# Performance work log

Measured on AMD Instinct MI355X. Metric: run time of the kernel, lower is better.

Reference implementation:

```python
import jax, jax.numpy as jnp
import numpy as np

B, T, H, N_IN, N_OUT = 256, 1024, 512, 64, 64


def setup_inputs() -> dict:
    key = jax.random.key(0)
    k_x, k_w, k_win, k_wout = jax.random.split(key, 4)
    # nn.Linear(in, out, bias=False) weight has shape [out, in]
    X = jax.random.normal(k_x, (B, T, N_IN), dtype=jnp.float32)
    h0 = jnp.zeros((B, H), dtype=jnp.float32)
    W = jax.random.normal(k_w, (H, H), dtype=jnp.float32) / np.sqrt(H)
    W_in = jax.random.normal(k_win, (H, N_IN), dtype=jnp.float32) / np.sqrt(N_IN)
    W_out = jax.random.normal(k_wout, (N_OUT, H), dtype=jnp.float32) / np.sqrt(H)
    return {"X": X, "h0": h0, "W": W, "W_in": W_in, "W_out": W_out}


def reference(X, h0, W, W_in, W_out):
    # Precompute input projections for all timesteps in one big GEMM:
    # inp[b, t, h] = X[b, t, :] @ W_in.T  (same math as per-step W_in(x_t))
    inp = jnp.einsum("bti,hi->tbh", X, W_in)  # [T, B, H]

    def step(h, inp_t):
        h_next = jnp.tanh(h) @ W.T + inp_t  # [B, H]
        return h_next, h_next

    _, hidden = jax.lax.scan(step, h0, inp)  # hidden: [T, B, H]
    hidden = jnp.transpose(hidden, (1, 0, 2))  # [B, T, H]
    out = jnp.einsum("bth,oh->bto", hidden, W_out)  # [B, T, n_out]
    return out, hidden
```

## Files before the change

kernel.cpp:

```cpp
#include <hip/hip_runtime.h>
#include <stdint.h>

#define B_    256
#define T_    1024
#define H_    512
#define NIN_  64
#define NOUT_ 64

#define SC_NW   8
#define BBLK    4
#define HROW    528
#define KB_REG  10
#define KB_STR  6
#define SW_CHUNKS (SC_NW * KB_STR * 4 * 64)

typedef __attribute__((ext_vector_type(8))) short bf16x8;
typedef __attribute__((ext_vector_type(4))) float f32x4;

__device__ __forceinline__ short f2bf(float f) {
  uint32_t u = __float_as_uint(f);
  uint32_t r = (u + 0x7FFFu + ((u >> 16) & 1u)) >> 16;
  return (short)(r & 0xFFFFu);
}

__device__ __forceinline__ bf16x8 pack8(float4 lo, float4 hi) {
  bf16x8 s;
  s[0] = f2bf(lo.x); s[1] = f2bf(lo.y); s[2] = f2bf(lo.z); s[3] = f2bf(lo.w);
  s[4] = f2bf(hi.x); s[5] = f2bf(hi.y); s[6] = f2bf(hi.z); s[7] = f2bf(hi.w);
  return s;
}

__device__ __forceinline__ float fast_tanh(float x) {
  float e = __expf(2.0f * x);
  return 1.0f - __fdividef(2.0f, e + 1.0f);
}

__global__ __launch_bounds__(512) void wprep(
    const float* __restrict__ W, short* __restrict__ sw)
{
  const int c = blockIdx.x * 512 + threadIdx.x;
  if (c >= SW_CHUNKS) return;
  const int lane = c & 63;
  const int u    = c >> 6;
  const int jt   = u & 3;
  const int gw   = u >> 2;
  const int G    = gw % KB_STR;
  const int w    = gw / KB_STR;
  const int col  = 64 * w + 16 * jt + (lane & 15);
  const int k0   = 32 * (KB_REG + G) + (lane >> 4) * 8;
  const float4* p = reinterpret_cast<const float4*>(W + (size_t)col * H_ + k0);
  *reinterpret_cast<bf16x8*>(sw + (size_t)c * 8) = pack8(p[0], p[1]);
}

#define XP_BLOCKS 512
__global__ __launch_bounds__(512, 2) void xproj(
    const float* __restrict__ X, const float* __restrict__ Win,
    float* __restrict__ inp)
{
  const int tid  = threadIdx.x;
  const int lane = tid & 63;
  const int w    = tid >> 6;
  const int g    = lane >> 4;
  const int m    = lane & 15;

  bf16x8 Bf[2][4];
#pragma unroll
  for (int kb = 0; kb < 2; ++kb)
#pragma unroll
    for (int jt = 0; jt < 4; ++jt) {
      const int j = 64 * w + 16 * jt + m;
      const float4* p = reinterpret_cast<const float4*>(Win + (size_t)j * NIN_ + 32 * kb + 8 * g);
      Bf[kb][jt] = pack8(p[0], p[1]);
    }

  const int NTILES = (B_ * T_) / 16;
  const f32x4 zero = {0.f, 0.f, 0.f, 0.f};

  for (int tile = blockIdx.x; tile < NTILES; tile += XP_BLOCKS) {
    const size_t row0 = (size_t)tile * 16;
    f32x4 acc[4];
    {
      const float4* p = reinterpret_cast<const float4*>(X + (row0 + m) * NIN_ + 8 * g);
      const bf16x8 a = pack8(p[0], p[1]);
#pragma unroll
      for (int jt = 0; jt < 4; ++jt)
        acc[jt] = __builtin_amdgcn_mfma_f32_16x16x32_bf16(a, Bf[0][jt], zero, 0, 0, 0);
    }
    {
      const float4* p = reinterpret_cast<const float4*>(X + (row0 + m) * NIN_ + 32 + 8 * g);
      const bf16x8 a = pack8(p[0], p[1]);
#pragma unroll
      for (int jt = 0; jt < 4; ++jt)
        acc[jt] = __builtin_amdgcn_mfma_f32_16x16x32_bf16(a, Bf[1][jt], acc[jt], 0, 0, 0);
    }
#pragma unroll
    for (int jt = 0; jt < 4; ++jt)
#pragma unroll
      for (int r = 0; r < 4; ++r)
        inp[(row0 + 4 * g + r) * H_ + 64 * w + 16 * jt + m] = acc[jt][r];
  }
}

__global__
__attribute__((amdgpu_flat_work_group_size(512, 512), amdgpu_waves_per_eu(2, 2)))
void rnn_scan(
    const float* __restrict__ h0, const float* __restrict__ W,
    float* __restrict__ hid, const short* __restrict__ swbuf)
{
  __shared__ __align__(16) short hbuf[2][BBLK][HROW];

  const int tid  = threadIdx.x;
  const int lane = tid & 63;
  const int w    = tid >> 6;
  const int g    = lane >> 4;
  const int m    = lane & 15;
  const int b0   = blockIdx.x * BBLK;

  bf16x8 Wf[KB_REG][4];
#pragma unroll
  for (int kb = 0; kb < KB_REG; ++kb)
#pragma unroll
    for (int jt = 0; jt < 4; ++jt) {
      const int col = 64 * w + 16 * jt + m;
      const float4* p = reinterpret_cast<const float4*>(W + (size_t)col * H_ + 32 * kb + 8 * g);
      Wf[kb][jt] = pack8(p[0], p[1]);
    }

  for (int e = tid; e < BBLK * H_; e += SC_NW * 64) {
    const int r = e >> 9, k = e & (H_ - 1);
    hbuf[0][r][k] = f2bf(fast_tanh(h0[(size_t)(b0 + r) * H_ + k]));
  }

  const int mycol = 64 * w + 16 * g + m;
  float inp_cur[4];
#pragma unroll
  for (int r = 0; r < 4; ++r)
    inp_cur[r] = hid[((size_t)(b0 + r) * T_ + 0) * H_ + mycol];

  const int sbase = (w * KB_STR * 4) * 64 + lane;
  const bf16x8* SW = reinterpret_cast<const bf16x8*>(swbuf);
  bf16x8 s0[4], s1[4];
#pragma unroll
  for (int jt = 0; jt < 4; ++jt) s0[jt] = SW[sbase + (0 * 4 + jt) * 64];
#pragma unroll
  for (int jt = 0; jt < 4; ++jt) s1[jt] = SW[sbase + (1 * 4 + jt) * 64];

  __syncthreads();

#pragma clang loop unroll(disable)
  for (int t = 0; t < T_; ++t) {
    const int cur = t & 1, nxt = cur ^ 1;

    uintptr_t swo_u = (uintptr_t)SW;
    asm volatile("" : "+s"(swo_u));
    const bf16x8* SWo = (const bf16x8*)swo_u;

    float inp_nxt[4] = {0.f, 0.f, 0.f, 0.f};
    if (t + 1 < T_) {
#pragma unroll
      for (int r = 0; r < 4; ++r)
        inp_nxt[r] = hid[((size_t)(b0 + r) * T_ + (t + 1)) * H_ + mycol];
    }

    const short* hr = &hbuf[cur][m & 3][0];
    f32x4 acc[4];
#pragma unroll
    for (int jt = 0; jt < 4; ++jt) acc[jt] = (f32x4){0.f, 0.f, 0.f, 0.f};

#pragma unroll
    for (int ph = 0; ph < 5; ++ph) {
#pragma unroll
      for (int kk = 0; kk < 2; ++kk) {
        const int kb = 2 * ph + kk;
        const bf16x8 a = *reinterpret_cast<const bf16x8*>(hr + 32 * kb + 8 * g);
#pragma unroll
        for (int jt = 0; jt < 4; ++jt)
          acc[jt] = __builtin_amdgcn_mfma_f32_16x16x32_bf16(a, Wf[kb][jt], acc[jt], 0, 0, 0);
      }
      if (ph < 4) {
        const bf16x8 a = *reinterpret_cast<const bf16x8*>(hr + 32 * (KB_REG + ph) + 8 * g);
        if ((ph & 1) == 0) {
#pragma unroll
          for (int jt = 0; jt < 4; ++jt)
            acc[jt] = __builtin_amdgcn_mfma_f32_16x16x32_bf16(a, s0[jt], acc[jt], 0, 0, 0);
#pragma unroll
          for (int jt = 0; jt < 4; ++jt) s0[jt] = SWo[sbase + ((ph + 2) * 4 + jt) * 64];
        } else {
#pragma unroll
          for (int jt = 0; jt < 4; ++jt)
            acc[jt] = __builtin_amdgcn_mfma_f32_16x16x32_bf16(a, s1[jt], acc[jt], 0, 0, 0);
#pragma unroll
          for (int jt = 0; jt < 4; ++jt) s1[jt] = SWo[sbase + ((ph + 2) * 4 + jt) * 64];
        }
      }
    }
    {
      const bf16x8 a = *reinterpret_cast<const bf16x8*>(hr + 32 * 14 + 8 * g);
#pragma unroll
      for (int jt = 0; jt < 4; ++jt)
        acc[jt] = __builtin_amdgcn_mfma_f32_16x16x32_bf16(a, s0[jt], acc[jt], 0, 0, 0);
    }
    {
      const bf16x8 a = *reinterpret_cast<const bf16x8*>(hr + 32 * 15 + 8 * g);
#pragma unroll
      for (int jt = 0; jt < 4; ++jt)
        acc[jt] = __builtin_amdgcn_mfma_f32_16x16x32_bf16(a, s1[jt], acc[jt], 0, 0, 0);
    }
#pragma unroll
    for (int jt = 0; jt < 4; ++jt) s0[jt] = SWo[sbase + (0 * 4 + jt) * 64];
#pragma unroll
    for (int jt = 0; jt < 4; ++jt) s1[jt] = SWo[sbase + (1 * 4 + jt) * 64];

#pragma unroll
    for (int r = 0; r < 4; ++r) {
      float v = acc[0][r];
      v = (g == 1) ? acc[1][r] : v;
      v = (g == 2) ? acc[2][r] : v;
      v = (g == 3) ? acc[3][r] : v;
      v += inp_cur[r];
      hid[((size_t)(b0 + r) * T_ + t) * H_ + mycol] = v;
      hbuf[nxt][r][mycol] = f2bf(fast_tanh(v));
    }
#pragma unroll
    for (int r = 0; r < 4; ++r) inp_cur[r] = inp_nxt[r];

    asm volatile("s_waitcnt lgkmcnt(0)" ::: "memory");
    __builtin_amdgcn_s_barrier();
    asm volatile("" ::: "memory");
  }
}

#define OP_BLOCKS 1024
#define OP_WAVES  8
__global__ __launch_bounds__(OP_WAVES * 64, 2) void out_proj(
    const float* __restrict__ hid, const float* __restrict__ Wout,
    float* __restrict__ out)
{
  __shared__ __align__(16) short ws[16][NOUT_][32];

  const int tid  = threadIdx.x;
  const int lane = tid & 63;
  const int w    = tid >> 6;
  const int g    = lane >> 4;
  const int m    = lane & 15;

#pragma unroll
  for (int i = 0; i < 8; ++i) {
    const int c   = tid + OP_WAVES * 64 * i;
    const int kb  = c >> 8;
    const int col = (c >> 2) & 63;
    const int q   = (c & 3) * 8;
    const float4* p = reinterpret_cast<const float4*>(Wout + (size_t)col * H_ + 32 * kb + q);
    *reinterpret_cast<bf16x8*>(&ws[kb][col][q]) = pack8(p[0], p[1]);
  }
  __syncthreads();

  const int wave_id = blockIdx.x * OP_WAVES + w;
  const int NWAVES  = OP_BLOCKS * OP_WAVES;
  const int NTILES  = (B_ * T_) / 16;

  for (int tile = wave_id; tile < NTILES; tile += NWAVES) {
    const size_t row0 = (size_t)tile * 16;
    f32x4 acc[4];
    {
      const float4* p = reinterpret_cast<const float4*>(hid + (row0 + m) * H_ + 8 * g);
      const bf16x8 a = pack8(p[0], p[1]);
      const f32x4 zero = {0.f, 0.f, 0.f, 0.f};
#pragma unroll
      for (int jt = 0; jt < 4; ++jt) {
        const bf16x8 b = *reinterpret_cast<const bf16x8*>(&ws[0][16 * jt + m][8 * g]);
        acc[jt] = __builtin_amdgcn_mfma_f32_16x16x32_bf16(a, b, zero, 0, 0, 0);
      }
    }
#pragma unroll
    for (int kb = 1; kb < 16; ++kb) {
      const float4* p = reinterpret_cast<const float4*>(hid + (row0 + m) * H_ + 32 * kb + 8 * g);
      const bf16x8 a = pack8(p[0], p[1]);
#pragma unroll
      for (int jt = 0; jt < 4; ++jt) {
        const bf16x8 b = *reinterpret_cast<const bf16x8*>(&ws[kb][16 * jt + m][8 * g]);
        acc[jt] = __builtin_amdgcn_mfma_f32_16x16x32_bf16(a, b, acc[jt], 0, 0, 0);
      }
    }
#pragma unroll
    for (int jt = 0; jt < 4; ++jt)
#pragma unroll
      for (int r = 0; r < 4; ++r)
        out[(row0 + 4 * g + r) * NOUT_ + 16 * jt + m] = acc[jt][r];
  }
}

extern "C" void kernel_launch(void* const* d_in, const int* in_sizes, int n_in,
                              void* d_out, int out_size, void* d_ws, size_t ws_size,
                              hipStream_t stream) {
  const float* X    = (const float*)d_in[0];
  const float* h0   = (const float*)d_in[1];
  const float* W    = (const float*)d_in[2];
  const float* Win  = (const float*)d_in[3];
  const float* Wout = (const float*)d_in[4];

  float* out = (float*)d_out;
  float* hid = (float*)d_out + (size_t)B_ * T_ * NOUT_;

  const size_t out_elems = (size_t)B_ * T_ * NOUT_;
  short* sw = (short*)((float*)d_out + out_elems) - (size_t)SW_CHUNKS * 8;

  wprep<<<dim3(SW_CHUNKS / 512), dim3(512), 0, stream>>>(W, sw);
  xproj<<<dim3(XP_BLOCKS), dim3(512), 0, stream>>>(X, Win, hid);
  rnn_scan<<<dim3(B_ / BBLK), dim3(SC_NW * 64), 0, stream>>>(h0, W, hid, sw);
  out_proj<<<dim3(OP_BLOCKS), dim3(OP_WAVES * 64), 0, stream>>>(hid, Wout, out);
}
```

Baseline: 2.925 ms.

## Split W operand across AGPRs, global streaming and LDS in scan loop

The per-step W operand storage is reorganized three ways. Eight k-blocks are held in AGPRs and consumed by inline-asm MFMAs, four are streamed from the prepacked global buffer with double-buffered registers, and four are staged once in LDS and read each step. Before, ten blocks sat in VGPRs and six were streamed from global. The goal is to cut global/L2 traffic per timestep and free VGPRs. In exchange it adds LDS reads competing with the hbuf reads, uses inline asm with an s_nop hazard pad, and changes the MFMA ordering.

```diff
diff --git a/kernel.cpp b/kernel.cpp
--- a/kernel.cpp
+++ b/kernel.cpp
@@ -10,9 +10,11 @@
 #define SC_NW   8
 #define BBLK    4
 #define HROW    528
-#define KB_REG  10
-#define KB_STR  6
-#define SW_CHUNKS (SC_NW * KB_STR * 4 * 64)
+#define KB_AG   8
+#define KB_ST   4
+#define KB_LD   4
+#define LD_U    (KB_LD * 4)
+#define SW_CHUNKS (SC_NW * KB_ST * 4 * 64)
 
 typedef __attribute__((ext_vector_type(8))) short bf16x8;
 typedef __attribute__((ext_vector_type(4))) float f32x4;
@@ -33,6 +35,19 @@
 __device__ __forceinline__ float fast_tanh(float x) {
   float e = __expf(2.0f * x);
   return 1.0f - __fdividef(2.0f, e + 1.0f);
+}
+
+__device__ __forceinline__ void mfma4_agpr(
+    f32x4& d0, f32x4& d1, f32x4& d2, f32x4& d3, bf16x8 a,
+    const bf16x8& b0, const bf16x8& b1, const bf16x8& b2, const bf16x8& b3) {
+  asm volatile(
+      "v_mfma_f32_16x16x32_bf16 %0, %4, %5, %0\n\t"
+      "v_mfma_f32_16x16x32_bf16 %1, %4, %6, %1\n\t"
+      "v_mfma_f32_16x16x32_bf16 %2, %4, %7, %2\n\t"
+      "v_mfma_f32_16x16x32_bf16 %3, %4, %8, %3\n\t"
+      "s_nop 7"
+      : "+v"(d0), "+v"(d1), "+v"(d2), "+v"(d3)
+      : "v"(a), "a"(b0), "a"(b1), "a"(b2), "a"(b3));
 }
 
 __global__ __launch_bounds__(512) void wprep(
@@ -44,10 +59,10 @@
   const int u    = c >> 6;
   const int jt   = u & 3;
   const int gw   = u >> 2;
-  const int G    = gw % KB_STR;
-  const int w    = gw / KB_STR;
+  const int G    = gw & 3;
+  const int w    = gw >> 2;
   const int col  = 64 * w + 16 * jt + (lane & 15);
-  const int k0   = 32 * (KB_REG + G) + (lane >> 4) * 8;
+  const int k0   = 32 * (KB_AG + G) + (lane >> 4) * 8;
   const float4* p = reinterpret_cast<const float4*>(W + (size_t)col * H_ + k0);
   *reinterpret_cast<bf16x8*>(sw + (size_t)c * 8) = pack8(p[0], p[1]);
 }
@@ -107,6 +122,7 @@
     const float* __restrict__ h0, const float* __restrict__ W,
     float* __restrict__ hid, const short* __restrict__ swbuf)
 {
+  __shared__ __align__(16) short wlds[SC_NW * LD_U * 64 * 8];
   __shared__ __align__(16) short hbuf[2][BBLK][HROW];
 
   const int tid  = threadIdx.x;
@@ -116,15 +132,34 @@
   const int m    = lane & 15;
   const int b0   = blockIdx.x * BBLK;
 
-  bf16x8 Wf[KB_REG][4];
-#pragma unroll
-  for (int kb = 0; kb < KB_REG; ++kb)
+  const float* Wo = W;
+  asm volatile("" : "+s"(Wo));
+  const short* SWb = swbuf;
+  asm volatile("" : "+s"(SWb));
+
+  bf16x8 Wa[KB_AG][4];
+#pragma unroll
+  for (int kb = 0; kb < KB_AG; ++kb)
 #pragma unroll
     for (int jt = 0; jt < 4; ++jt) {
       const int col = 64 * w + 16 * jt + m;
-      const float4* p = reinterpret_cast<const float4*>(W + (size_t)col * H_ + 32 * kb + 8 * g);
-      Wf[kb][jt] = pack8(p[0], p[1]);
-    }
+      const float4* p = reinterpret_cast<const float4*>(Wo + (size_t)col * H_ + 32 * kb + 8 * g);
+      Wa[kb][jt] = pack8(p[0], p[1]);
+    }
+
+#pragma unroll
+  for (int i = 0; i < 16; ++i) {
+    const int c  = tid + 512 * i;
+    const int l  = c & 63;
+    const int u  = (c >> 6) & 15;
+    const int ww = c >> 10;
+    const int kb = 12 + (u >> 2);
+    const int jt = u & 3;
+    const int col = 64 * ww + 16 * jt + (l & 15);
+    const int k0  = 32 * kb + (l >> 4) * 8;
+    const float4* p = reinterpret_cast<const float4*>(Wo + (size_t)col * H_ + k0);
+    *reinterpret_cast<bf16x8*>(&wlds[((size_t)(ww * LD_U + u) * 64 + l) * 8]) = pack8(p[0], p[1]);
+  }
 
   for (int e = tid; e < BBLK * H_; e += SC_NW * 64) {
     const int r = e >> 9, k = e & (H_ - 1);
@@ -137,13 +172,13 @@
   for (int r = 0; r < 4; ++r)
     inp_cur[r] = hid[((size_t)(b0 + r) * T_ + 0) * H_ + mycol];
 
-  const int sbase = (w * KB_STR * 4) * 64 + lane;
-  const bf16x8* SW = reinterpret_cast<const bf16x8*>(swbuf);
-  bf16x8 s0[4], s1[4];
-#pragma unroll
-  for (int jt = 0; jt < 4; ++jt) s0[jt] = SW[sbase + (0 * 4 + jt) * 64];
-#pragma unroll
-  for (int jt = 0; jt < 4; ++jt) s1[jt] = SW[sbase + (1 * 4 + jt) * 64];
+  const int sbase = (w * KB_ST * 4) * 64 + lane;
+  const bf16x8* SW = reinterpret_cast<const bf16x8*>(SWb);
+  bf16x8 sb0[4], sb1[4];
+#pragma unroll
+  for (int jt = 0; jt < 4; ++jt) sb0[jt] = SW[sbase + (0 * 4 + jt) * 64];
+#pragma unroll
+  for (int jt = 0; jt < 4; ++jt) sb1[jt] = SW[sbase + (1 * 4 + jt) * 64];
 
   __syncthreads();
 
@@ -164,52 +199,74 @@
 
     const short* hr = &hbuf[cur][m & 3][0];
     f32x4 acc[4];
-#pragma unroll
-    for (int jt = 0; jt < 4; ++jt) acc[jt] = (f32x4){0.f, 0.f, 0.f, 0.f};
-
-#pragma unroll
-    for (int ph = 0; ph < 5; ++ph) {
-#pragma unroll
-      for (int kk = 0; kk < 2; ++kk) {
-        const int kb = 2 * ph + kk;
-        const bf16x8 a = *reinterpret_cast<const bf16x8*>(hr + 32 * kb + 8 * g);
-#pragma unroll
-        for (int jt = 0; jt < 4; ++jt)
-          acc[jt] = __builtin_amdgcn_mfma_f32_16x16x32_bf16(a, Wf[kb][jt], acc[jt], 0, 0, 0);
+
+    {
+      const bf16x8 a = *reinterpret_cast<const bf16x8*>(hr + 32 * 8 + 8 * g);
+      const f32x4 zero = {0.f, 0.f, 0.f, 0.f};
+#pragma unroll
+      for (int jt = 0; jt < 4; ++jt)
+        acc[jt] = __builtin_amdgcn_mfma_f32_16x16x32_bf16(a, sb0[jt], zero, 0, 0, 0);
+#pragma unroll
+      for (int jt = 0; jt < 4; ++jt) sb0[jt] = SWo[sbase + (2 * 4 + jt) * 64];
+    }
+
+#pragma unroll
+    for (int kb = 0; kb < KB_AG; ++kb) {
+      const bf16x8 a = *reinterpret_cast<const bf16x8*>(hr + 32 * kb + 8 * g);
+      mfma4_agpr(acc[0], acc[1], acc[2], acc[3], a,
+                 Wa[kb][0], Wa[kb][1], Wa[kb][2], Wa[kb][3]);
+    }
+
+    {
+      const bf16x8 a = *reinterpret_cast<const bf16x8*>(hr + 32 * 9 + 8 * g);
+#pragma unroll
+      for (int jt = 0; jt < 4; ++jt)
+        acc[jt] = __builtin_amdgcn_mfma_f32_16x16x32_bf16(a, sb1[jt], acc[jt], 0, 0, 0);
+#pragma unroll
+      for (int jt = 0; jt < 4; ++jt) sb1[jt] = SWo[sbase + (3 * 4 + jt) * 64];
+    }
+
+#pragma unroll
+    for (int kk = 0; kk < 2; ++kk) {
+      const int kb = 12 + kk;
+      const bf16x8 a = *reinterpret_cast<const bf16x8*>(hr + 32 * kb + 8 * g);
+#pragma unroll
+      for (int jt = 0; jt < 4; ++jt) {
+        const bf16x8 b = *reinterpret_cast<const bf16x8*>(
+            &wlds[((size_t)(w * LD_U + kk * 4 + jt) * 64 + lane) * 8]);
+        acc[jt] = __builtin_amdgcn_mfma_f32_16x16x32_bf16(a, b, acc[jt], 0, 0, 0);
       }
-      if (ph < 4) {
-        const bf16x8 a = *reinterpret_cast<const bf16x8*>(hr + 32 * (KB_REG + ph) + 8 * g);
-        if ((ph & 1) == 0) {
-#pragma unroll
-          for (int jt = 0; jt < 4; ++jt)
-            acc[jt] = __builtin_amdgcn_mfma_f32_16x16x32_bf16(a, s0[jt], acc[jt], 0, 0, 0);
-#pragma unroll
-          for (int jt = 0; jt < 4; ++jt) s0[jt] = SWo[sbase + ((ph + 2) * 4 + jt) * 64];
-        } else {
-#pragma unroll
-          for (int jt = 0; jt < 4; ++jt)
-            acc[jt] = __builtin_amdgcn_mfma_f32_16x16x32_bf16(a, s1[jt], acc[jt], 0, 0, 0);
-#pragma unroll
-          for (int jt = 0; jt < 4; ++jt) s1[jt] = SWo[sbase + ((ph + 2) * 4 + jt) * 64];
-        }
+    }
+
+    {
+      const bf16x8 a = *reinterpret_cast<const bf16x8*>(hr + 32 * 10 + 8 * g);
+#pragma unroll
+      for (int jt = 0; jt < 4; ++jt)
+        acc[jt] = __builtin_amdgcn_mfma_f32_16x16x32_bf16(a, sb0[jt], acc[jt], 0, 0, 0);
+#pragma unroll
+      for (int jt = 0; jt < 4; ++jt) sb0[jt] = SWo[sbase + (0 * 4 + jt) * 64];
+    }
+
+#pragma unroll
+    for (int kk = 2; kk < 4; ++kk) {
+      const int kb = 12 + kk;
+      const bf16x8 a = *reinterpret_cast<const bf16x8*>(hr + 32 * kb + 8 * g);
+#pragma unroll
+      for (int jt = 0; jt < 4; ++jt) {
+        const bf16x8 b = *reinterpret_cast<const bf16x8*>(
+            &wlds[((size_t)(w * LD_U + kk * 4 + jt) * 64 + lane) * 8]);
+        acc[jt] = __builtin_amdgcn_mfma_f32_16x16x32_bf16(a, b, acc[jt], 0, 0, 0);
       }
     }
-    {
-      const bf16x8 a = *reinterpret_cast<const bf16x8*>(hr + 32 * 14 + 8 * g);
-#pragma unroll
-      for (int jt = 0; jt < 4; ++jt)
-        acc[jt] = __builtin_amdgcn_mfma_f32_16x16x32_bf16(a, s0[jt], acc[jt], 0, 0, 0);
-    }
-    {
-      const bf16x8 a = *reinterpret_cast<const bf16x8*>(hr + 32 * 15 + 8 * g);
-#pragma unroll
-      for (int jt = 0; jt < 4; ++jt)
-        acc[jt] = __builtin_amdgcn_mfma_f32_16x16x32_bf16(a, s1[jt], acc[jt], 0, 0, 0);
-    }
-#pragma unroll
-    for (int jt = 0; jt < 4; ++jt) s0[jt] = SWo[sbase + (0 * 4 + jt) * 64];
-#pragma unroll
-    for (int jt = 0; jt < 4; ++jt) s1[jt] = SWo[sbase + (1 * 4 + jt) * 64];
+
+    {
+      const bf16x8 a = *reinterpret_cast<const bf16x8*>(hr + 32 * 11 + 8 * g);
+#pragma unroll
+      for (int jt = 0; jt < 4; ++jt)
+        acc[jt] = __builtin_amdgcn_mfma_f32_16x16x32_bf16(a, sb1[jt], acc[jt], 0, 0, 0);
+#pragma unroll
+      for (int jt = 0; jt < 4; ++jt) sb1[jt] = SWo[sbase + (1 * 4 + jt) * 64];
+    }
 
 #pragma unroll
     for (int r = 0; r < 4; ++r) {
```

Result: faster. 2.855 ms (-2.4%).
